# Kernel tuning notes

Measured on AMD Instinct MI355X. Metric: run time of the kernel, lower is better.

Reference implementation:

```python
import jax, jax.numpy as jnp
import numpy as np

B, T, D = 2, 2048, 1024
G, E, F = 4, 4, 4096          # num_groups, experts_per_group, d_ff
KG, KE = 2, 1                  # top_k_groups, top_k_experts


def setup_inputs() -> dict:
    key = jax.random.key(0)
    ks = jax.random.split(key, 5)
    init = lambda k, shape, fan: jax.random.normal(k, shape, jnp.float32) / np.sqrt(fan).astype(np.float32)
    x = jax.random.normal(ks[0], (B, T, D), jnp.float32)
    Wg = init(ks[1], (G, D), D)          # group router (torch Linear weight [out,in])
    We = init(ks[2], (G, E, D), D)       # per-group expert routers
    W1 = init(ks[3], (G, E, F, D), D)    # expert up-proj weights
    W2 = init(ks[4], (G, E, D, F), F)    # expert down-proj weights
    return {"x": x, "Wg": Wg, "We": We, "W1": W1, "W2": W2}


def _moe_forward(x, Wg, We, W1, W2):
    b, t, d = x.shape
    xf = x.reshape(b * t, d)                                   # [N, D]
    group_logits = xf @ Wg.T                                   # [N, G]
    gw, gid = jax.lax.top_k(group_logits, KG)                  # [N, KG]
    gw = jax.nn.softmax(gw, axis=-1)
    expert_logits = jnp.einsum('nd,ged->nge', xf, We)          # [N, G, E]
    sel = jnp.take_along_axis(expert_logits, gid[:, :, None], axis=1)  # [N, KG, E]
    ew, eid = jax.lax.top_k(sel, KE)                           # [N, KG, KE]
    ew = jax.nn.softmax(ew, axis=-1)
    w = gw[:, :, None] * ew                                    # [N, KG, KE]
    oh_g = jax.nn.one_hot(gid, G, dtype=xf.dtype)              # [N, KG, G]
    oh_e = jax.nn.one_hot(eid, E, dtype=xf.dtype)              # [N, KG, KE, E]
    # topk group ids are distinct, and expert ids within a group are distinct,
    # so this scatter-by-one-hot exactly reproduces the masked accumulation.
    combine = jnp.einsum('nrg,nrke,nrk->nge', oh_g, oh_e, w)   # [N, G, E]
    out = jnp.zeros_like(xf)
    for g in range(G):
        for e in range(E):
            h = jax.nn.gelu(xf @ W1[g, e].T, approximate=False)  # exact GELU, as nn.GELU()
            out = out + combine[:, g, e, None] * (h @ W2[g, e].T)
    return out.reshape(b, t, d), group_logits.reshape(b, t, G)


def reference(x, Wg, We, W1, W2):
    out, group_logits = _moe_forward(x, Wg, We, W1, W2)
    p = jax.nn.softmax(group_logits, axis=-1)
    lp = jax.nn.log_softmax(group_logits, axis=-1)
    group_entropy = -(p * lp).sum(-1).mean()
    return out, group_logits, group_entropy
```

## Files before the change

kernel.cpp:

```cpp
#include <hip/hip_runtime.h>
#include <hip/hip_bf16.h>

#define NTOK 4096
#define DDIM 1024
#define GG 4
#define EE 4
#define FF 4096
#define NEXP 16
#define OUT_ELEMS 4194304
#define GL_OFF 4194304
#define ENT_OFF 4210688

typedef float f32x4 __attribute__((ext_vector_type(4)));
typedef short short8 __attribute__((ext_vector_type(8)));

__device__ inline unsigned short f2bf(float f) {
  unsigned int u = __float_as_uint(f);
  unsigned int rounding = 0x7FFFu + ((u >> 16) & 1u);
  return (unsigned short)((u + rounding) >> 16);
}
__device__ inline unsigned int pack2(float f0, float f1) {
  return (unsigned int)f2bf(f0) | ((unsigned int)f2bf(f1) << 16);
}
__device__ inline unsigned int pack2rn(float f0, float f1) {
  unsigned int u0 = __float_as_uint(f0), u1 = __float_as_uint(f1);
  return ((u0 + 0x8000u) >> 16) | ((u1 + 0x8000u) & 0xFFFF0000u);
}

__device__ __forceinline__ void gload_lds16(const void* g, void* l) {
  __builtin_amdgcn_global_load_lds(
      (const __attribute__((address_space(1))) unsigned int*)g,
      (__attribute__((address_space(3))) unsigned int*)l, 16, 0, 0);
}

__global__ void cvt_kernel(const float* __restrict__ x, unsigned short* __restrict__ xb) {
  int idx = blockIdx.x * 256 + threadIdx.x;
  const float4* p = reinterpret_cast<const float4*>(x) + (size_t)idx * 2;
  float4 a = p[0], b = p[1];
  uint4 v;
  v.x = pack2(a.x, a.y); v.y = pack2(a.z, a.w);
  v.z = pack2(b.x, b.y); v.w = pack2(b.z, b.w);
  reinterpret_cast<uint4*>(xb)[idx] = v;
}

__global__ __launch_bounds__(256) void routing_kernel(
    const float* __restrict__ x, const float* __restrict__ Wg,
    const float* __restrict__ We, float* __restrict__ out,
    int* __restrict__ cnt, int* __restrict__ tokL, int* __restrict__ hrwL,
    float* __restrict__ wslot) {
  int wave = threadIdx.x >> 6, lane = threadIdx.x & 63;
  int token = blockIdx.x * 4 + wave;
  const float4* xr = reinterpret_cast<const float4*>(x + (size_t)token * DDIM);
  float4 xv[4];
#pragma unroll
  for (int c = 0; c < 4; c++) xv[c] = xr[c * 64 + lane];

  auto dotrow = [&](const float* w) -> float {
    const float4* w4 = reinterpret_cast<const float4*>(w);
    float s = 0.f;
#pragma unroll
    for (int c = 0; c < 4; c++) {
      float4 wv = w4[c * 64 + lane];
      s += xv[c].x * wv.x + xv[c].y * wv.y + xv[c].z * wv.z + xv[c].w * wv.w;
    }
#pragma unroll
    for (int off = 32; off; off >>= 1) s += __shfl_xor(s, off, 64);
    return s;
  };

  float gl[GG];
#pragma unroll
  for (int g = 0; g < GG; g++) gl[g] = dotrow(Wg + g * DDIM);

  int g0 = 0;
  for (int g = 1; g < GG; g++) if (gl[g] > gl[g0]) g0 = g;
  int g1 = -1;
  for (int g = 0; g < GG; g++) { if (g == g0) continue; if (g1 < 0 || gl[g] > gl[g1]) g1 = g; }
  float e1 = __expf(gl[g1] - gl[g0]);
  float inv = 1.f / (1.f + e1);
  float w0 = inv, w1 = e1 * inv;

  int gsel[2] = {g0, g1};
  float wsel[2] = {w0, w1};
  int esel[2];
#pragma unroll
  for (int r = 0; r < 2; r++) {
    float el[EE];
#pragma unroll
    for (int e = 0; e < EE; e++) el[e] = dotrow(We + ((size_t)gsel[r] * EE + e) * DDIM);
    int best = 0;
    for (int e = 1; e < EE; e++) if (el[e] > el[best]) best = e;
    esel[r] = best;
  }

  float m = gl[0];
  for (int g = 1; g < GG; g++) m = fmaxf(m, gl[g]);
  float se = 0.f;
  for (int g = 0; g < GG; g++) se += __expf(gl[g] - m);
  float lse = __logf(se);
  float ent = 0.f;
  for (int g = 0; g < GG; g++) {
    float lp = gl[g] - m - lse;
    ent -= __expf(lp) * lp;
  }

  if (lane == 0) {
    for (int g = 0; g < GG; g++) out[GL_OFF + token * GG + g] = gl[g];
    atomicAdd(out + ENT_OFF, ent * (1.0f / NTOK));
    for (int r = 0; r < 2; r++) {
      int ge = gsel[r] * EE + esel[r];
      int pos = atomicAdd(cnt + ge, 1);
      tokL[ge * NTOK + pos] = token;
      hrwL[ge * NTOK + pos] = r * NTOK + token;
      wslot[r * NTOK + token] = wsel[r];
    }
  }
}

__global__ __launch_bounds__(256) void up_kernel(
    const unsigned short* __restrict__ xb, const float* __restrict__ W1,
    const int* __restrict__ cnt, const int* __restrict__ tokL,
    const int* __restrict__ hrwL, unsigned short* __restrict__ H) {
  int ge = blockIdx.z, mt = blockIdx.y;
  int count = cnt[ge];
  if (mt * 128 >= count) return;
  int f0 = blockIdx.x * 128;

  __shared__ unsigned short As[128 * 32];
  __shared__ unsigned short Bs[128 * 32];
  __shared__ int rowsS[128];
  __shared__ int destS[128];

  int t = threadIdx.x;
  int w = t >> 6, lane = t & 63;
  if (t < 128) {
    int i = mt * 128 + t;
    bool valid = i < count;
    rowsS[t] = valid ? tokL[ge * NTOK + i] : 0;
    destS[t] = valid ? hrwL[ge * NTOK + i] : -1;
  }
  __syncthreads();

  int r0 = w * 16 + (lane >> 2);
  const unsigned short* a0 = xb + (size_t)rowsS[r0] * DDIM + (lane & 3) * 8;
  const unsigned short* a1 = xb + (size_t)rowsS[r0 + 64] * DDIM + (lane & 3) * 8;
  unsigned short* l0 = &As[w * 512];
  unsigned short* l1 = &As[2048 + w * 512];

  const float* bsrc = W1 + ((size_t)ge * FF + (f0 + (t >> 1))) * DDIM + (t & 1) * 16;
  unsigned short* bdst = &Bs[(t >> 1) * 32 + (t & 1) * 16];

  int m0 = (w >> 1) * 64, n0w = (w & 1) * 64;
  int kg = (lane >> 4) * 8;
  int rl = lane & 15;

  f32x4 acc[4][4] = {};

  for (int kb = 0; kb < DDIM; kb += 32) {
    gload_lds16(a0 + kb, l0);
    gload_lds16(a1 + kb, l1);
    float4 q0 = *reinterpret_cast<const float4*>(bsrc + kb);
    float4 q1 = *reinterpret_cast<const float4*>(bsrc + kb + 4);
    float4 q2 = *reinterpret_cast<const float4*>(bsrc + kb + 8);
    float4 q3 = *reinterpret_cast<const float4*>(bsrc + kb + 12);
    uint4 v0, v1;
    v0.x = pack2rn(q0.x, q0.y); v0.y = pack2rn(q0.z, q0.w);
    v0.z = pack2rn(q1.x, q1.y); v0.w = pack2rn(q1.z, q1.w);
    v1.x = pack2rn(q2.x, q2.y); v1.y = pack2rn(q2.z, q2.w);
    v1.z = pack2rn(q3.x, q3.y); v1.w = pack2rn(q3.z, q3.w);
    *reinterpret_cast<uint4*>(bdst) = v0;
    *reinterpret_cast<uint4*>(bdst + 8) = v1;
    __syncthreads();
    short8 af[4];
#pragma unroll
    for (int i = 0; i < 4; i++)
      af[i] = *reinterpret_cast<const short8*>(&As[(m0 + i * 16 + rl) * 32 + kg]);
#pragma unroll
    for (int j = 0; j < 4; j++) {
      short8 bf = *reinterpret_cast<const short8*>(&Bs[(n0w + j * 16 + rl) * 32 + kg]);
#pragma unroll
      for (int i = 0; i < 4; i++)
        acc[i][j] = __builtin_amdgcn_mfma_f32_16x16x32_bf16(af[i], bf, acc[i][j], 0, 0, 0);
    }
    __syncthreads();
  }

  int re = (lane >> 4) * 4;
#pragma unroll
  for (int i = 0; i < 4; i++) {
#pragma unroll
    for (int e = 0; e < 4; e++) {
      int hr = destS[m0 + i * 16 + re + e];
      if (hr >= 0) {
#pragma unroll
        for (int j = 0; j < 4; j++) {
          float v = acc[i][j][e];
          float gel = 0.5f * v * (1.0f + erff(v * 0.70710678118654752f));
          H[(size_t)hr * FF + f0 + n0w + j * 16 + rl] = f2bf(gel);
        }
      }
    }
  }
}

__global__ __launch_bounds__(256) void down_kernel(
    const unsigned short* __restrict__ H, const float* __restrict__ W2,
    const int* __restrict__ cnt, const int* __restrict__ hrwL,
    float* __restrict__ Y) {
  int ge = blockIdx.z, mt = blockIdx.y;
  int count = cnt[ge];
  if (mt * 128 >= count) return;
  int d0 = blockIdx.x * 128;

  __shared__ unsigned short As[128 * 32];
  __shared__ unsigned short Bs[128 * 32];
  __shared__ int rowsS[128];

  int t = threadIdx.x;
  int w = t >> 6, lane = t & 63;
  if (t < 128) {
    int i = mt * 128 + t;
    bool valid = i < count;
    rowsS[t] = valid ? hrwL[ge * NTOK + i] : -1;
  }
  __syncthreads();

  int r0 = w * 16 + (lane >> 2);
  int ar0 = rowsS[r0] < 0 ? 0 : rowsS[r0];
  int ar1 = rowsS[r0 + 64] < 0 ? 0 : rowsS[r0 + 64];
  const unsigned short* a0 = H + (size_t)ar0 * FF + (lane & 3) * 8;
  const unsigned short* a1 = H + (size_t)ar1 * FF + (lane & 3) * 8;
  unsigned short* l0 = &As[w * 512];
  unsigned short* l1 = &As[2048 + w * 512];

  const float* bsrc = W2 + ((size_t)ge * DDIM + (d0 + (t >> 1))) * FF + (t & 1) * 16;
  unsigned short* bdst = &Bs[(t >> 1) * 32 + (t & 1) * 16];

  int m0 = (w >> 1) * 64, n0w = (w & 1) * 64;
  int kg = (lane >> 4) * 8;
  int rl = lane & 15;

  f32x4 acc[4][4] = {};

  for (int kb = 0; kb < FF; kb += 32) {
    gload_lds16(a0 + kb, l0);
    gload_lds16(a1 + kb, l1);
    float4 q0 = *reinterpret_cast<const float4*>(bsrc + kb);
    float4 q1 = *reinterpret_cast<const float4*>(bsrc + kb + 4);
    float4 q2 = *reinterpret_cast<const float4*>(bsrc + kb + 8);
    float4 q3 = *reinterpret_cast<const float4*>(bsrc + kb + 12);
    uint4 v0, v1;
    v0.x = pack2rn(q0.x, q0.y); v0.y = pack2rn(q0.z, q0.w);
    v0.z = pack2rn(q1.x, q1.y); v0.w = pack2rn(q1.z, q1.w);
    v1.x = pack2rn(q2.x, q2.y); v1.y = pack2rn(q2.z, q2.w);
    v1.z = pack2rn(q3.x, q3.y); v1.w = pack2rn(q3.z, q3.w);
    *reinterpret_cast<uint4*>(bdst) = v0;
    *reinterpret_cast<uint4*>(bdst + 8) = v1;
    __syncthreads();
    short8 af[4];
#pragma unroll
    for (int i = 0; i < 4; i++)
      af[i] = *reinterpret_cast<const short8*>(&As[(m0 + i * 16 + rl) * 32 + kg]);
#pragma unroll
    for (int j = 0; j < 4; j++) {
      short8 bf = *reinterpret_cast<const short8*>(&Bs[(n0w + j * 16 + rl) * 32 + kg]);
#pragma unroll
      for (int i = 0; i < 4; i++)
        acc[i][j] = __builtin_amdgcn_mfma_f32_16x16x32_bf16(af[i], bf, acc[i][j], 0, 0, 0);
    }
    __syncthreads();
  }

  int re = (lane >> 4) * 4;
#pragma unroll
  for (int i = 0; i < 4; i++) {
#pragma unroll
    for (int e = 0; e < 4; e++) {
      int hr = rowsS[m0 + i * 16 + re + e];
      if (hr >= 0) {
#pragma unroll
        for (int j = 0; j < 4; j++) {
          Y[(size_t)hr * DDIM + d0 + n0w + j * 16 + rl] = acc[i][j][e];
        }
      }
    }
  }
}

__global__ void combine_kernel(const float* __restrict__ Y,
                               const float* __restrict__ wslot,
                               float* __restrict__ out) {
  int idx = blockIdx.x * 256 + threadIdx.x;
  int token = idx >> 8;
  float w0 = wslot[token], w1 = wslot[NTOK + token];
  float4 a = reinterpret_cast<const float4*>(Y)[idx];
  float4 b = reinterpret_cast<const float4*>(Y + (size_t)NTOK * DDIM)[idx];
  float4 o;
  o.x = w0 * a.x + w1 * b.x;
  o.y = w0 * a.y + w1 * b.y;
  o.z = w0 * a.z + w1 * b.z;
  o.w = w0 * a.w + w1 * b.w;
  reinterpret_cast<float4*>(out)[idx] = o;
}

extern "C" void kernel_launch(void* const* d_in, const int* in_sizes, int n_in,
                              void* d_out, int out_size, void* d_ws, size_t ws_size,
                              hipStream_t stream) {
  const float* x  = (const float*)d_in[0];
  const float* Wg = (const float*)d_in[1];
  const float* We = (const float*)d_in[2];
  const float* W1 = (const float*)d_in[3];
  const float* W2 = (const float*)d_in[4];
  float* out = (float*)d_out;
  char* ws = (char*)d_ws;

  int* cnt = (int*)(ws);
  int* tokL = (int*)(ws + 1024);
  int* hrwL = (int*)(ws + 1024 + 262144);
  float* wslot = (float*)(ws + 1024 + 524288);
  unsigned short* xb = (unsigned short*)(ws + (1 << 20));
  unsigned short* H  = (unsigned short*)(ws + (1 << 20) + 8388608);
  float* Y = (float*)(ws + (1 << 20) + 8388608 + 67108864);

  hipMemsetAsync(d_out, 0, (size_t)out_size * sizeof(float), stream);
  hipMemsetAsync(ws, 0, 1024, stream);

  cvt_kernel<<<2048, 256, 0, stream>>>(x, xb);
  routing_kernel<<<1024, 256, 0, stream>>>(x, Wg, We, out, cnt, tokL, hrwL, wslot);
  up_kernel<<<dim3(FF / 128, 32, NEXP), 256, 0, stream>>>(xb, W1, cnt, tokL, hrwL, H);
  down_kernel<<<dim3(DDIM / 128, 32, NEXP), 256, 0, stream>>>(H, W2, cnt, hrwL, Y);
  combine_kernel<<<4096, 256, 0, stream>>>(Y, wslot, out);
}
```

Before: 1.004 ms.

## Merge expert GEMMs into templated double-buffered kernel with swizzled LDS

Replaces the separate up and down expert GEMM kernels with one templated kernel that uses 512 threads, a K-step of 64, and double-buffered LDS tiles. The next tile's global loads (A via direct-to-LDS, B as fp32 converted to bf16) are issued before the MFMAs on the current tile, and the converted B is written to LDS afterwards. This overlaps memory latency with compute and halves the number of barriers. An XOR swizzle on LDS columns aims to cut bank conflicts. In exchange it uses four times the LDS per block and a smaller per-wave tile (32x64), which may hurt occupancy or per-wave MFMA reuse.

```diff
diff --git a/kernel.cpp b/kernel.cpp
--- a/kernel.cpp
+++ b/kernel.cpp
@@ -117,170 +117,129 @@
   }
 }
 
-__global__ __launch_bounds__(256) void up_kernel(
-    const unsigned short* __restrict__ xb, const float* __restrict__ W1,
+template <int KDIM, bool UP>
+__global__ __launch_bounds__(512, 4) void moe_gemm(
+    const unsigned short* __restrict__ A, const float* __restrict__ W,
     const int* __restrict__ cnt, const int* __restrict__ tokL,
-    const int* __restrict__ hrwL, unsigned short* __restrict__ H) {
+    const int* __restrict__ hrwL, unsigned short* __restrict__ Hout,
+    float* __restrict__ Yout) {
+  constexpr int NT = KDIM / 64;
+  constexpr int NROWS = UP ? FF : DDIM;
   int ge = blockIdx.z, mt = blockIdx.y;
   int count = cnt[ge];
   if (mt * 128 >= count) return;
-  int f0 = blockIdx.x * 128;
-
-  __shared__ unsigned short As[128 * 32];
-  __shared__ unsigned short Bs[128 * 32];
-  __shared__ int rowsS[128];
-  __shared__ int destS[128];
+  int n0 = blockIdx.x * 128;
+
+  __shared__ alignas(16) unsigned short As[2][128 * 64];
+  __shared__ alignas(16) unsigned short Bs[2][128 * 64];
+  __shared__ int srcS[128];
+  __shared__ int dstS[128];
 
   int t = threadIdx.x;
   int w = t >> 6, lane = t & 63;
   if (t < 128) {
     int i = mt * 128 + t;
     bool valid = i < count;
-    rowsS[t] = valid ? tokL[ge * NTOK + i] : 0;
-    destS[t] = valid ? hrwL[ge * NTOK + i] : -1;
+    int hrw = valid ? hrwL[ge * NTOK + i] : -1;
+    dstS[t] = hrw;
+    if (UP) srcS[t] = valid ? tokL[ge * NTOK + i] : 0;
+    else    srcS[t] = hrw < 0 ? 0 : hrw;
   }
   __syncthreads();
 
-  int r0 = w * 16 + (lane >> 2);
-  const unsigned short* a0 = xb + (size_t)rowsS[r0] * DDIM + (lane & 3) * 8;
-  const unsigned short* a1 = xb + (size_t)rowsS[r0 + 64] * DDIM + (lane & 3) * 8;
-  unsigned short* l0 = &As[w * 512];
-  unsigned short* l1 = &As[2048 + w * 512];
-
-  const float* bsrc = W1 + ((size_t)ge * FF + (f0 + (t >> 1))) * DDIM + (t & 1) * 16;
-  unsigned short* bdst = &Bs[(t >> 1) * 32 + (t & 1) * 16];
-
-  int m0 = (w >> 1) * 64, n0w = (w & 1) * 64;
-  int kg = (lane >> 4) * 8;
-  int rl = lane & 15;
-
-  f32x4 acc[4][4] = {};
-
-  for (int kb = 0; kb < DDIM; kb += 32) {
-    gload_lds16(a0 + kb, l0);
-    gload_lds16(a1 + kb, l1);
-    float4 q0 = *reinterpret_cast<const float4*>(bsrc + kb);
-    float4 q1 = *reinterpret_cast<const float4*>(bsrc + kb + 4);
-    float4 q2 = *reinterpret_cast<const float4*>(bsrc + kb + 8);
-    float4 q3 = *reinterpret_cast<const float4*>(bsrc + kb + 12);
+  int rA = w * 16 + (lane >> 3);
+  int cA = (lane & 7) ^ (lane >> 3);
+  const unsigned short* gA0 = A + (size_t)srcS[rA] * KDIM + cA * 8;
+  const unsigned short* gA1 = A + (size_t)srcS[rA + 8] * KDIM + cA * 8;
+
+  int rB = t >> 3;
+  int cB = t & 7;
+  const float* gB0 = W + ((size_t)ge * NROWS + n0 + rB) * KDIM + cB * 8;
+  const float* gB1 = W + ((size_t)ge * NROWS + n0 + 64 + rB) * KDIM + cB * 8;
+  int pB = (cB ^ (rB & 7)) * 8;
+
+  int wr = w >> 1, wc = w & 1;
+  int m0 = wr * 32, nw = wc * 64;
+  int rl = lane & 15, kq = lane >> 4;
+  int xr = rl & 7;
+
+  f32x4 acc[2][4] = {};
+  int cur = 0;
+
+  {
+    gload_lds16(gA0, &As[0][(w * 16) * 64]);
+    gload_lds16(gA1, &As[0][(w * 16 + 8) * 64]);
+    float4 q0 = *reinterpret_cast<const float4*>(gB0);
+    float4 q1 = *reinterpret_cast<const float4*>(gB0 + 4);
+    float4 q2 = *reinterpret_cast<const float4*>(gB1);
+    float4 q3 = *reinterpret_cast<const float4*>(gB1 + 4);
     uint4 v0, v1;
     v0.x = pack2rn(q0.x, q0.y); v0.y = pack2rn(q0.z, q0.w);
     v0.z = pack2rn(q1.x, q1.y); v0.w = pack2rn(q1.z, q1.w);
     v1.x = pack2rn(q2.x, q2.y); v1.y = pack2rn(q2.z, q2.w);
     v1.z = pack2rn(q3.x, q3.y); v1.w = pack2rn(q3.z, q3.w);
-    *reinterpret_cast<uint4*>(bdst) = v0;
-    *reinterpret_cast<uint4*>(bdst + 8) = v1;
+    *reinterpret_cast<uint4*>(&Bs[0][rB * 64 + pB]) = v0;
+    *reinterpret_cast<uint4*>(&Bs[0][(rB + 64) * 64 + pB]) = v1;
+  }
+  __syncthreads();
+
+  for (int it = 0; it < NT; ++it) {
+    int kb = (it + 1) * 64;
+    bool pre = (it + 1) < NT;
+    float4 q0, q1, q2, q3;
+    if (pre) {
+      gload_lds16(gA0 + kb, &As[cur ^ 1][(w * 16) * 64]);
+      gload_lds16(gA1 + kb, &As[cur ^ 1][(w * 16 + 8) * 64]);
+      q0 = *reinterpret_cast<const float4*>(gB0 + kb);
+      q1 = *reinterpret_cast<const float4*>(gB0 + kb + 4);
+      q2 = *reinterpret_cast<const float4*>(gB1 + kb);
+      q3 = *reinterpret_cast<const float4*>(gB1 + kb + 4);
+    }
+    const unsigned short* Ab = As[cur];
+    const unsigned short* Bb = Bs[cur];
+#pragma unroll
+    for (int kk = 0; kk < 2; kk++) {
+      int cph = ((kk * 4 + kq) ^ xr) * 8;
+      short8 af0 = *reinterpret_cast<const short8*>(&Ab[(m0 + rl) * 64 + cph]);
+      short8 af1 = *reinterpret_cast<const short8*>(&Ab[(m0 + 16 + rl) * 64 + cph]);
+#pragma unroll
+      for (int j = 0; j < 4; j++) {
+        short8 bf = *reinterpret_cast<const short8*>(&Bb[(nw + j * 16 + rl) * 64 + cph]);
+        acc[0][j] = __builtin_amdgcn_mfma_f32_16x16x32_bf16(af0, bf, acc[0][j], 0, 0, 0);
+        acc[1][j] = __builtin_amdgcn_mfma_f32_16x16x32_bf16(af1, bf, acc[1][j], 0, 0, 0);
+      }
+    }
+    if (pre) {
+      uint4 v0, v1;
+      v0.x = pack2rn(q0.x, q0.y); v0.y = pack2rn(q0.z, q0.w);
+      v0.z = pack2rn(q1.x, q1.y); v0.w = pack2rn(q1.z, q1.w);
+      v1.x = pack2rn(q2.x, q2.y); v1.y = pack2rn(q2.z, q2.w);
+      v1.z = pack2rn(q3.x, q3.y); v1.w = pack2rn(q3.z, q3.w);
+      *reinterpret_cast<uint4*>(&Bs[cur ^ 1][rB * 64 + pB]) = v0;
+      *reinterpret_cast<uint4*>(&Bs[cur ^ 1][(rB + 64) * 64 + pB]) = v1;
+    }
     __syncthreads();
-    short8 af[4];
-#pragma unroll
-    for (int i = 0; i < 4; i++)
-      af[i] = *reinterpret_cast<const short8*>(&As[(m0 + i * 16 + rl) * 32 + kg]);
-#pragma unroll
-    for (int j = 0; j < 4; j++) {
-      short8 bf = *reinterpret_cast<const short8*>(&Bs[(n0w + j * 16 + rl) * 32 + kg]);
-#pragma unroll
-      for (int i = 0; i < 4; i++)
-        acc[i][j] = __builtin_amdgcn_mfma_f32_16x16x32_bf16(af[i], bf, acc[i][j], 0, 0, 0);
-    }
-    __syncthreads();
-  }
-
-  int re = (lane >> 4) * 4;
-#pragma unroll
-  for (int i = 0; i < 4; i++) {
+    cur ^= 1;
+  }
+
+  int re = kq * 4;
+#pragma unroll
+  for (int i = 0; i < 2; i++) {
 #pragma unroll
     for (int e = 0; e < 4; e++) {
-      int hr = destS[m0 + i * 16 + re + e];
+      int hr = dstS[m0 + i * 16 + re + e];
       if (hr >= 0) {
-#pragma unroll
-        for (int j = 0; j < 4; j++) {
-          float v = acc[i][j][e];
-          float gel = 0.5f * v * (1.0f + erff(v * 0.70710678118654752f));
-          H[(size_t)hr * FF + f0 + n0w + j * 16 + rl] = f2bf(gel);
-        }
-      }
-    }
-  }
-}
-
-__global__ __launch_bounds__(256) void down_kernel(
-    const unsigned short* __restrict__ H, const float* __restrict__ W2,
-    const int* __restrict__ cnt, const int* __restrict__ hrwL,
-    float* __restrict__ Y) {
-  int ge = blockIdx.z, mt = blockIdx.y;
-  int count = cnt[ge];
-  if (mt * 128 >= count) return;
-  int d0 = blockIdx.x * 128;
-
-  __shared__ unsigned short As[128 * 32];
-  __shared__ unsigned short Bs[128 * 32];
-  __shared__ int rowsS[128];
-
-  int t = threadIdx.x;
-  int w = t >> 6, lane = t & 63;
-  if (t < 128) {
-    int i = mt * 128 + t;
-    bool valid = i < count;
-    rowsS[t] = valid ? hrwL[ge * NTOK + i] : -1;
-  }
-  __syncthreads();
-
-  int r0 = w * 16 + (lane >> 2);
-  int ar0 = rowsS[r0] < 0 ? 0 : rowsS[r0];
-  int ar1 = rowsS[r0 + 64] < 0 ? 0 : rowsS[r0 + 64];
-  const unsigned short* a0 = H + (size_t)ar0 * FF + (lane & 3) * 8;
-  const unsigned short* a1 = H + (size_t)ar1 * FF + (lane & 3) * 8;
-  unsigned short* l0 = &As[w * 512];
-  unsigned short* l1 = &As[2048 + w * 512];
-
-  const float* bsrc = W2 + ((size_t)ge * DDIM + (d0 + (t >> 1))) * FF + (t & 1) * 16;
-  unsigned short* bdst = &Bs[(t >> 1) * 32 + (t & 1) * 16];
-
-  int m0 = (w >> 1) * 64, n0w = (w & 1) * 64;
-  int kg = (lane >> 4) * 8;
-  int rl = lane & 15;
-
-  f32x4 acc[4][4] = {};
-
-  for (int kb = 0; kb < FF; kb += 32) {
-    gload_lds16(a0 + kb, l0);
-    gload_lds16(a1 + kb, l1);
-    float4 q0 = *reinterpret_cast<const float4*>(bsrc + kb);
-    float4 q1 = *reinterpret_cast<const float4*>(bsrc + kb + 4);
-    float4 q2 = *reinterpret_cast<const float4*>(bsrc + kb + 8);
-    float4 q3 = *reinterpret_cast<const float4*>(bsrc + kb + 12);
-    uint4 v0, v1;
-    v0.x = pack2rn(q0.x, q0.y); v0.y = pack2rn(q0.z, q0.w);
-    v0.z = pack2rn(q1.x, q1.y); v0.w = pack2rn(q1.z, q1.w);
-    v1.x = pack2rn(q2.x, q2.y); v1.y = pack2rn(q2.z, q2.w);
-    v1.z = pack2rn(q3.x, q3.y); v1.w = pack2rn(q3.z, q3.w);
-    *reinterpret_cast<uint4*>(bdst) = v0;
-    *reinterpret_cast<uint4*>(bdst + 8) = v1;
-    __syncthreads();
-    short8 af[4];
-#pragma unroll
-    for (int i = 0; i < 4; i++)
-      af[i] = *reinterpret_cast<const short8*>(&As[(m0 + i * 16 + rl) * 32 + kg]);
-#pragma unroll
-    for (int j = 0; j < 4; j++) {
-      short8 bf = *reinterpret_cast<const short8*>(&Bs[(n0w + j * 16 + rl) * 32 + kg]);
-#pragma unroll
-      for (int i = 0; i < 4; i++)
-        acc[i][j] = __builtin_amdgcn_mfma_f32_16x16x32_bf16(af[i], bf, acc[i][j], 0, 0, 0);
-    }
-    __syncthreads();
-  }
-
-  int re = (lane >> 4) * 4;
-#pragma unroll
-  for (int i = 0; i < 4; i++) {
-#pragma unroll
-    for (int e = 0; e < 4; e++) {
-      int hr = rowsS[m0 + i * 16 + re + e];
-      if (hr >= 0) {
-#pragma unroll
-        for (int j = 0; j < 4; j++) {
-          Y[(size_t)hr * DDIM + d0 + n0w + j * 16 + rl] = acc[i][j][e];
+        if constexpr (UP) {
+#pragma unroll
+          for (int j = 0; j < 4; j++) {
+            float v = acc[i][j][e];
+            float gel = 0.5f * v * (1.0f + erff(v * 0.70710678118654752f));
+            Hout[(size_t)hr * FF + n0 + nw + j * 16 + rl] = f2bf(gel);
+          }
+        } else {
+#pragma unroll
+          for (int j = 0; j < 4; j++)
+            Yout[(size_t)hr * DDIM + n0 + nw + j * 16 + rl] = acc[i][j][e];
         }
       }
     }
@@ -327,7 +286,9 @@
 
   cvt_kernel<<<2048, 256, 0, stream>>>(x, xb);
   routing_kernel<<<1024, 256, 0, stream>>>(x, Wg, We, out, cnt, tokL, hrwL, wslot);
-  up_kernel<<<dim3(FF / 128, 32, NEXP), 256, 0, stream>>>(xb, W1, cnt, tokL, hrwL, H);
-  down_kernel<<<dim3(DDIM / 128, 32, NEXP), 256, 0, stream>>>(H, W2, cnt, hrwL, Y);
+  moe_gemm<DDIM, true><<<dim3(FF / 128, 32, NEXP), 512, 0, stream>>>(
+      xb, W1, cnt, tokL, hrwL, H, nullptr);
+  moe_gemm<FF, false><<<dim3(DDIM / 128, 32, NEXP), 512, 0, stream>>>(
+      H, W2, cnt, tokL, hrwL, nullptr, Y);
   combine_kernel<<<4096, 256, 0, stream>>>(Y, wslot, out);
 }
```

New measurement: 915.9 us. -8.7%, faster.
